# Optimization experiments

Hardware: AMD Instinct MI355X
Metric: run time of the kernel (lower is better)

Reference implementation:

```python
import jax, jax.numpy as jnp
import numpy as np


def _gen_grid(rotations, size):
    # Replicates _Volume.VolumeGenGrid(U^T, grid): rotate normalized voxel coords.
    # grid[b,d,h,w,:] = R^T @ [x_w, y_h, z_d], components ordered (x,y,z) for grid_sample.
    c = jnp.linspace(-1.0, 1.0, size, dtype=jnp.float32)
    zz, yy, xx = jnp.meshgrid(c, c, c, indexing='ij')      # [S,S,S] each (d,h,w)
    base = jnp.stack([xx, yy, zz], axis=-1)                 # [S,S,S,3]
    UT = jnp.swapaxes(rotations, 1, 2)                      # [B,3,3]
    return jnp.einsum('bij,dhwj->bdhwi', UT, base)          # [B,S,S,S,3]


def _grid_sample_3d(vol, grid):
    # Trilinear grid_sample, padding_mode='zeros', align_corners=False (torch default).
    B, C, D, H, W = vol.shape
    x = (grid[..., 0] + 1.0) * W * 0.5 - 0.5
    y = (grid[..., 1] + 1.0) * H * 0.5 - 0.5
    z = (grid[..., 2] + 1.0) * D * 0.5 - 0.5
    x0 = jnp.floor(x); y0 = jnp.floor(y); z0 = jnp.floor(z)
    tx = x - x0; ty = y - y0; tz = z - z0
    vol_flat = vol.reshape(B, C, D * H * W)
    out = jnp.zeros(vol.shape, dtype=vol.dtype)
    for dz in (0, 1):
        for dy in (0, 1):
            for dx in (0, 1):
                xi = x0 + dx; yi = y0 + dy; zi = z0 + dz
                w = (jnp.where(dx, tx, 1.0 - tx)
                     * jnp.where(dy, ty, 1.0 - ty)
                     * jnp.where(dz, tz, 1.0 - tz))
                valid = ((xi >= 0) & (xi < W) & (yi >= 0) & (yi < H)
                         & (zi >= 0) & (zi < D))
                xi_c = jnp.clip(xi, 0, W - 1).astype(jnp.int32)
                yi_c = jnp.clip(yi, 0, H - 1).astype(jnp.int32)
                zi_c = jnp.clip(zi, 0, D - 1).astype(jnp.int32)
                lin = (zi_c * H + yi_c) * W + xi_c              # [B,S,S,S]
                lin = lin.reshape(B, 1, -1)
                g = jnp.take_along_axis(vol_flat, jnp.broadcast_to(lin, (B, C, lin.shape[-1])), axis=2)
                wm = (w * valid.astype(vol.dtype)).reshape(B, 1, -1)
                out = out + (g * wm).reshape(vol.shape)
    return out


def setup_inputs() -> dict:
    key = jax.random.key(0)
    k1, k2 = jax.random.split(key)
    B, C, S = 8, 16, 64
    input_volume = jax.random.normal(k1, (B, C, S, S, S), dtype=jnp.float32)
    A = jax.random.normal(k2, (B, 3, 3), dtype=jnp.float32)
    Q, _ = jnp.linalg.qr(A)                                  # orthonormal rotations
    rotations = Q.astype(jnp.float32)
    return {"input_volume": input_volume, "rotations": rotations}


def reference(input_volume, rotations):
    size = input_volume.shape[2]
    grid = _gen_grid(rotations, size)
    return _grid_sample_3d(input_volume, grid)
```

## Files before the change

### kernel.cpp

```cpp
#include <hip/hip_runtime.h>


#define S 64
#define SP (S * S * S)
#define CCH 16
#define BB 8

#define TW 16
#define TH 8
#define TD 8
#define NT 512
#define PPT 2
#define CAP 8192
#define MAXIT 16

__global__ __launch_bounds__(NT, 4) void vol_rot_tiled(
    const float* __restrict__ vol,
    const float* __restrict__ rot,
    float* __restrict__ out)
{
    __shared__ float smem[CAP + 2];

    const int tid = threadIdx.x;
    const int t  = blockIdx.x & 255;
    const int b  = blockIdx.x >> 8;
    const int w0 = (t & 3) * TW;
    const int h0 = ((t >> 2) & 7) * TH;
    const int d0 = (t >> 5) * TD;

    const float* R = rot + b * 9;
    const float R00 = R[0], R01 = R[1], R02 = R[2];
    const float R10 = R[3], R11 = R[4], R12 = R[5];
    const float R20 = R[6], R21 = R[7], R22 = R[8];

    const float st = 2.0f / 63.0f;

    float xmn = 1e30f, xmx = -1e30f;
    float ymn = 1e30f, ymx = -1e30f;
    float zmn = 1e30f, zmx = -1e30f;
#pragma unroll
    for (int k = 0; k < 8; ++k) {
        const float xb = -1.0f + (float)(w0 + ((k & 1) ? (TW - 1) : 0)) * st;
        const float yb = -1.0f + (float)(h0 + ((k & 2) ? (TH - 1) : 0)) * st;
        const float zb = -1.0f + (float)(d0 + ((k & 4) ? (TD - 1) : 0)) * st;
        const float gx = R00 * xb + R10 * yb + R20 * zb;
        const float gy = R01 * xb + R11 * yb + R21 * zb;
        const float gz = R02 * xb + R12 * yb + R22 * zb;
        const float vx = (gx + 1.0f) * 32.0f - 0.5f;
        const float vy = (gy + 1.0f) * 32.0f - 0.5f;
        const float vz = (gz + 1.0f) * 32.0f - 0.5f;
        xmn = fminf(xmn, vx); xmx = fmaxf(xmx, vx);
        ymn = fminf(ymn, vy); ymx = fmaxf(ymx, vy);
        zmn = fminf(zmn, vz); zmx = fmaxf(zmx, vz);
    }
    const int rx0 = (int)floorf(xmn);
    const int ry0 = (int)floorf(ymn);
    const int rz0 = (int)floorf(zmn);
    int ex = (int)floorf(xmx) + 2 - rx0;
    int ey = (int)floorf(ymx) + 2 - ry0;
    int ez = (int)floorf(zmx) + 2 - rz0;
    if (ex * ey * ez > CAP) ez = CAP / (ex * ey);

    const int plane = ex * ey;
    const float invp = 1.0f / (float)plane;
    const float inve = 1.0f / (float)ex;

    int voff[MAXIT];
    unsigned mask = 0;
#pragma unroll
    for (int i = 0; i < MAXIT; ++i) {
        const int r  = tid + i * NT;
        const int rz = (int)(((float)r + 0.5f) * invp);
        const int rm = r - rz * plane;
        const int ry = (int)(((float)rm + 0.5f) * inve);
        const int rx = rm - ry * ex;
        const int gx = rx0 + rx, gy = ry0 + ry, gz = rz0 + rz;
        const bool valid = ((unsigned)gx < 64u) & ((unsigned)gy < 64u)
                         & ((unsigned)gz < 64u);
        const int gxc = min(max(gx, 0), 63);
        const int gyc = min(max(gy, 0), 63);
        const int gzc = min(max(gz, 0), 63);
        voff[i] = (((((gzc << 6) + gyc) << 6) + gxc) << 2);
        mask |= ((unsigned)valid) << i;
    }

    int   obase[PPT];
    int   ospat[PPT];
    float wgt[PPT][8];
#pragma unroll
    for (int p = 0; p < PPT; ++p) {
        const int idx = tid + p * NT;
        const int pw = idx & 15, ph = (idx >> 4) & 7, pd = idx >> 7;
        const float xb = -1.0f + (float)(w0 + pw) * st;
        const float yb = -1.0f + (float)(h0 + ph) * st;
        const float zb = -1.0f + (float)(d0 + pd) * st;
        const float gx = R00 * xb + R10 * yb + R20 * zb;
        const float gy = R01 * xb + R11 * yb + R21 * zb;
        const float gz = R02 * xb + R12 * yb + R22 * zb;
        const float vx = (gx + 1.0f) * 32.0f - 0.5f;
        const float vy = (gy + 1.0f) * 32.0f - 0.5f;
        const float vz = (gz + 1.0f) * 32.0f - 0.5f;
        const float fx = floorf(vx), fy = floorf(vy), fz = floorf(vz);
        const float tx = vx - fx, ty = vy - fy, tz = vz - fz;
        int lx = (int)fx - rx0, ly = (int)fy - ry0, lz = (int)fz - rz0;
        lx = min(max(lx, 0), ex - 2);
        ly = min(max(ly, 0), ey - 2);
        lz = min(max(lz, 0), ez - 2);
        obase[p] = ((lz * ey + ly) * ex + lx) * 4;
        ospat[p] = ((d0 + pd) * 64 + (h0 + ph)) * 64 + (w0 + pw);
        const float ux = 1.0f - tx, uy = 1.0f - ty, uz = 1.0f - tz;
        wgt[p][0] = uz * uy * ux; wgt[p][1] = uz * uy * tx;
        wgt[p][2] = uz * ty * ux; wgt[p][3] = uz * ty * tx;
        wgt[p][4] = tz * uy * ux; wgt[p][5] = tz * uy * tx;
        wgt[p][6] = tz * ty * ux; wgt[p][7] = tz * ty * tx;
    }

    const char* smemb = (const char*)smem;
    const int dy4 = ex * 4;
    const int dz4 = plane * 4;
    const float* volb = vol + (size_t)b * CCH * SP;
    float*       outb = out + (size_t)b * CCH * SP;

    float vals[MAXIT];
    {
        const char* vc = (const char*)volb;
#pragma unroll
        for (int i = 0; i < MAXIT; ++i)
            vals[i] = *(const float*)(vc + voff[i]);
    }

    for (int c = 0; c < CCH; ++c) {
        __syncthreads();
#pragma unroll
        for (int i = 0; i < MAXIT; ++i) {
            const float v = ((mask >> i) & 1u) ? vals[i] : 0.0f;
            smem[tid + i * NT] = v;
        }
        __syncthreads();

        if (c + 1 < CCH) {
            const char* vc = (const char*)(volb + (c + 1) * SP);
#pragma unroll
            for (int i = 0; i < MAXIT; ++i)
                vals[i] = *(const float*)(vc + voff[i]);
        }

#pragma unroll
        for (int p = 0; p < PPT; ++p) {
            const char* pb = smemb + obase[p];
            const float v000 = *(const float*)(pb);
            const float v001 = *(const float*)(pb + 4);
            const float v010 = *(const float*)(pb + dy4);
            const float v011 = *(const float*)(pb + dy4 + 4);
            const float v100 = *(const float*)(pb + dz4);
            const float v101 = *(const float*)(pb + dz4 + 4);
            const float v110 = *(const float*)(pb + dz4 + dy4);
            const float v111 = *(const float*)(pb + dz4 + dy4 + 4);
            const float acc = wgt[p][0] * v000 + wgt[p][1] * v001
                            + wgt[p][2] * v010 + wgt[p][3] * v011
                            + wgt[p][4] * v100 + wgt[p][5] * v101
                            + wgt[p][6] * v110 + wgt[p][7] * v111;
            outb[c * SP + ospat[p]] = acc;
        }
    }
}

extern "C" void kernel_launch(void* const* d_in, const int* in_sizes, int n_in,
                              void* d_out, int out_size, void* d_ws, size_t ws_size,
                              hipStream_t stream) {
    const float* vol = (const float*)d_in[0];
    const float* rot = (const float*)d_in[1];
    float* out = (float*)d_out;

    vol_rot_tiled<<<dim3(BB * 256), dim3(NT), 0, stream>>>(vol, rot, out);
}
```

Measured before the change: 358.8 us.

## Replace LDS-staged tile with direct global gathers and XCD-aware block remap

Drops the shared-memory staging of each rotated source bounding box and its two barriers per channel. Each thread now precomputes its eight clamped corner offsets and zero-padding-aware weights, then gathers directly from global memory for every channel, relying on L1/L2 caches for reuse. The block index is remapped so neighbouring tiles of the same batch land on the same XCD, and launch bounds are raised to allow more resident workgroups. This trades explicit LDS reuse and coalesced staging loads for scattered cached global loads, which risks more memory traffic if cache hit rates are poor.

```diff
diff --git a/kernel.cpp b/kernel.cpp
--- a/kernel.cpp
+++ b/kernel.cpp
@@ -11,19 +11,17 @@
 #define TD 8
 #define NT 512
 #define PPT 2
-#define CAP 8192
-#define MAXIT 16
 
-__global__ __launch_bounds__(NT, 4) void vol_rot_tiled(
+__global__ __launch_bounds__(NT, 8) void vol_rot_gather(
     const float* __restrict__ vol,
     const float* __restrict__ rot,
     float* __restrict__ out)
 {
-    __shared__ float smem[CAP + 2];
+    const int tid = threadIdx.x;
 
-    const int tid = threadIdx.x;
-    const int t  = blockIdx.x & 255;
-    const int b  = blockIdx.x >> 8;
+    const int wg = (blockIdx.x & 7) * (BB * 256 / 8) + (blockIdx.x >> 3);
+    const int t  = wg & 255;
+    const int b  = wg >> 8;
     const int w0 = (t & 3) * TW;
     const int h0 = ((t >> 2) & 7) * TH;
     const int d0 = (t >> 5) * TD;
@@ -35,56 +33,7 @@
 
     const float st = 2.0f / 63.0f;
 
-    float xmn = 1e30f, xmx = -1e30f;
-    float ymn = 1e30f, ymx = -1e30f;
-    float zmn = 1e30f, zmx = -1e30f;
-#pragma unroll
-    for (int k = 0; k < 8; ++k) {
-        const float xb = -1.0f + (float)(w0 + ((k & 1) ? (TW - 1) : 0)) * st;
-        const float yb = -1.0f + (float)(h0 + ((k & 2) ? (TH - 1) : 0)) * st;
-        const float zb = -1.0f + (float)(d0 + ((k & 4) ? (TD - 1) : 0)) * st;
-        const float gx = R00 * xb + R10 * yb + R20 * zb;
-        const float gy = R01 * xb + R11 * yb + R21 * zb;
-        const float gz = R02 * xb + R12 * yb + R22 * zb;
-        const float vx = (gx + 1.0f) * 32.0f - 0.5f;
-        const float vy = (gy + 1.0f) * 32.0f - 0.5f;
-        const float vz = (gz + 1.0f) * 32.0f - 0.5f;
-        xmn = fminf(xmn, vx); xmx = fmaxf(xmx, vx);
-        ymn = fminf(ymn, vy); ymx = fmaxf(ymx, vy);
-        zmn = fminf(zmn, vz); zmx = fmaxf(zmx, vz);
-    }
-    const int rx0 = (int)floorf(xmn);
-    const int ry0 = (int)floorf(ymn);
-    const int rz0 = (int)floorf(zmn);
-    int ex = (int)floorf(xmx) + 2 - rx0;
-    int ey = (int)floorf(ymx) + 2 - ry0;
-    int ez = (int)floorf(zmx) + 2 - rz0;
-    if (ex * ey * ez > CAP) ez = CAP / (ex * ey);
-
-    const int plane = ex * ey;
-    const float invp = 1.0f / (float)plane;
-    const float inve = 1.0f / (float)ex;
-
-    int voff[MAXIT];
-    unsigned mask = 0;
-#pragma unroll
-    for (int i = 0; i < MAXIT; ++i) {
-        const int r  = tid + i * NT;
-        const int rz = (int)(((float)r + 0.5f) * invp);
-        const int rm = r - rz * plane;
-        const int ry = (int)(((float)rm + 0.5f) * inve);
-        const int rx = rm - ry * ex;
-        const int gx = rx0 + rx, gy = ry0 + ry, gz = rz0 + rz;
-        const bool valid = ((unsigned)gx < 64u) & ((unsigned)gy < 64u)
-                         & ((unsigned)gz < 64u);
-        const int gxc = min(max(gx, 0), 63);
-        const int gyc = min(max(gy, 0), 63);
-        const int gzc = min(max(gz, 0), 63);
-        voff[i] = (((((gzc << 6) + gyc) << 6) + gxc) << 2);
-        mask |= ((unsigned)valid) << i;
-    }
-
-    int   obase[PPT];
+    int   off[PPT][8];
     int   ospat[PPT];
     float wgt[PPT][8];
 #pragma unroll
@@ -102,66 +51,65 @@
         const float vz = (gz + 1.0f) * 32.0f - 0.5f;
         const float fx = floorf(vx), fy = floorf(vy), fz = floorf(vz);
         const float tx = vx - fx, ty = vy - fy, tz = vz - fz;
-        int lx = (int)fx - rx0, ly = (int)fy - ry0, lz = (int)fz - rz0;
-        lx = min(max(lx, 0), ex - 2);
-        ly = min(max(ly, 0), ey - 2);
-        lz = min(max(lz, 0), ez - 2);
-        obase[p] = ((lz * ey + ly) * ex + lx) * 4;
+        const int x0 = (int)fx, y0 = (int)fy, z0 = (int)fz;
+
+        const float wx0 = (1.0f - tx) * (((unsigned)x0       < 64u) ? 1.0f : 0.0f);
+        const float wx1 = tx          * (((unsigned)(x0 + 1) < 64u) ? 1.0f : 0.0f);
+        const float wy0 = (1.0f - ty) * (((unsigned)y0       < 64u) ? 1.0f : 0.0f);
+        const float wy1 = ty          * (((unsigned)(y0 + 1) < 64u) ? 1.0f : 0.0f);
+        const float wz0 = (1.0f - tz) * (((unsigned)z0       < 64u) ? 1.0f : 0.0f);
+        const float wz1 = tz          * (((unsigned)(z0 + 1) < 64u) ? 1.0f : 0.0f);
+
+        const int xc0 = min(max(x0,     0), 63);
+        const int xc1 = min(max(x0 + 1, 0), 63);
+        const int yc0 = min(max(y0,     0), 63);
+        const int yc1 = min(max(y0 + 1, 0), 63);
+        const int zc0 = min(max(z0,     0), 63);
+        const int zc1 = min(max(z0 + 1, 0), 63);
+
+        const int ry0b = yc0 << 6, ry1b = yc1 << 6;
+        const int pz0b = zc0 << 12, pz1b = zc1 << 12;
+        off[p][0] = (pz0b + ry0b + xc0) << 2;
+        off[p][1] = (pz0b + ry0b + xc1) << 2;
+        off[p][2] = (pz0b + ry1b + xc0) << 2;
+        off[p][3] = (pz0b + ry1b + xc1) << 2;
+        off[p][4] = (pz1b + ry0b + xc0) << 2;
+        off[p][5] = (pz1b + ry0b + xc1) << 2;
+        off[p][6] = (pz1b + ry1b + xc0) << 2;
+        off[p][7] = (pz1b + ry1b + xc1) << 2;
+
+        wgt[p][0] = wz0 * wy0 * wx0; wgt[p][1] = wz0 * wy0 * wx1;
+        wgt[p][2] = wz0 * wy1 * wx0; wgt[p][3] = wz0 * wy1 * wx1;
+        wgt[p][4] = wz1 * wy0 * wx0; wgt[p][5] = wz1 * wy0 * wx1;
+        wgt[p][6] = wz1 * wy1 * wx0; wgt[p][7] = wz1 * wy1 * wx1;
+
         ospat[p] = ((d0 + pd) * 64 + (h0 + ph)) * 64 + (w0 + pw);
-        const float ux = 1.0f - tx, uy = 1.0f - ty, uz = 1.0f - tz;
-        wgt[p][0] = uz * uy * ux; wgt[p][1] = uz * uy * tx;
-        wgt[p][2] = uz * ty * ux; wgt[p][3] = uz * ty * tx;
-        wgt[p][4] = tz * uy * ux; wgt[p][5] = tz * uy * tx;
-        wgt[p][6] = tz * ty * ux; wgt[p][7] = tz * ty * tx;
     }
 
-    const char* smemb = (const char*)smem;
-    const int dy4 = ex * 4;
-    const int dz4 = plane * 4;
-    const float* volb = vol + (size_t)b * CCH * SP;
-    float*       outb = out + (size_t)b * CCH * SP;
+    const float* vp = vol + (size_t)b * CCH * SP;
+    float*       op = out + (size_t)b * CCH * SP;
 
-    float vals[MAXIT];
-    {
-        const char* vc = (const char*)volb;
-#pragma unroll
-        for (int i = 0; i < MAXIT; ++i)
-            vals[i] = *(const float*)(vc + voff[i]);
-    }
-
+#pragma unroll 2
     for (int c = 0; c < CCH; ++c) {
-        __syncthreads();
-#pragma unroll
-        for (int i = 0; i < MAXIT; ++i) {
-            const float v = ((mask >> i) & 1u) ? vals[i] : 0.0f;
-            smem[tid + i * NT] = v;
-        }
-        __syncthreads();
-
-        if (c + 1 < CCH) {
-            const char* vc = (const char*)(volb + (c + 1) * SP);
-#pragma unroll
-            for (int i = 0; i < MAXIT; ++i)
-                vals[i] = *(const float*)(vc + voff[i]);
-        }
-
+        const char* vc = (const char*)vp;
 #pragma unroll
         for (int p = 0; p < PPT; ++p) {
-            const char* pb = smemb + obase[p];
-            const float v000 = *(const float*)(pb);
-            const float v001 = *(const float*)(pb + 4);
-            const float v010 = *(const float*)(pb + dy4);
-            const float v011 = *(const float*)(pb + dy4 + 4);
-            const float v100 = *(const float*)(pb + dz4);
-            const float v101 = *(const float*)(pb + dz4 + 4);
-            const float v110 = *(const float*)(pb + dz4 + dy4);
-            const float v111 = *(const float*)(pb + dz4 + dy4 + 4);
-            const float acc = wgt[p][0] * v000 + wgt[p][1] * v001
-                            + wgt[p][2] * v010 + wgt[p][3] * v011
-                            + wgt[p][4] * v100 + wgt[p][5] * v101
-                            + wgt[p][6] * v110 + wgt[p][7] * v111;
-            outb[c * SP + ospat[p]] = acc;
+            const float v0 = *(const float*)(vc + off[p][0]);
+            const float v1 = *(const float*)(vc + off[p][1]);
+            const float v2 = *(const float*)(vc + off[p][2]);
+            const float v3 = *(const float*)(vc + off[p][3]);
+            const float v4 = *(const float*)(vc + off[p][4]);
+            const float v5 = *(const float*)(vc + off[p][5]);
+            const float v6 = *(const float*)(vc + off[p][6]);
+            const float v7 = *(const float*)(vc + off[p][7]);
+            const float acc = wgt[p][0] * v0 + wgt[p][1] * v1
+                            + wgt[p][2] * v2 + wgt[p][3] * v3
+                            + wgt[p][4] * v4 + wgt[p][5] * v5
+                            + wgt[p][6] * v6 + wgt[p][7] * v7;
+            op[ospat[p]] = acc;
         }
+        vp += SP;
+        op += SP;
     }
 }
 
@@ -172,5 +120,5 @@
     const float* rot = (const float*)d_in[1];
     float* out = (float*)d_out;
 
-    vol_rot_tiled<<<dim3(BB * 256), dim3(NT), 0, stream>>>(vol, rot, out);
+    vol_rot_gather<<<dim3(BB * 256), dim3(NT), 0, stream>>>(vol, rot, out);
 }
```

New measurement: 793.3 us. 2.21x slower.
